# Optimization experiments

Measured on AMD Instinct MI355X. Metric: run time of the kernel, lower is better.

## Reference

```python
import jax, jax.numpy as jnp
import numpy as np

B, N, D = 2, 4096, 512
H, DH = 8, 64  # heads, dim_head; inner_dim = H*DH = 512
SCALE = DH ** -0.5


def setup_inputs() -> dict:
    key = jax.random.key(0)
    ks = jax.random.split(key, 5)
    s = 0.02
    return {
        "x": jax.random.normal(ks[0], (B, N, D), dtype=jnp.float32),
        "Wq": jax.random.normal(ks[1], (D, H * DH), dtype=jnp.float32) * s,
        "Wk": jax.random.normal(ks[2], (D, H * DH), dtype=jnp.float32) * s,
        "Wv": jax.random.normal(ks[3], (D, H * DH), dtype=jnp.float32) * s,
        "Wo": jax.random.normal(ks[4], (H * DH, D), dtype=jnp.float32) * s,
        "bo": jnp.zeros((D,), dtype=jnp.float32),
    }


def reference(x, Wq, Wk, Wv, Wo, bo):
    b, n, _ = x.shape
    # projections (bias-free), then split heads: b n (h d) -> b h n d
    q = (x @ Wq).reshape(b, n, H, DH).transpose(0, 2, 1, 3)
    k = (x @ Wk).reshape(b, n, H, DH).transpose(0, 2, 1, 3)
    v = (x @ Wv).reshape(b, n, H, DH).transpose(0, 2, 1, 3)
    # fp32 QK^T (module upcasts under ATTN_PRECISION='fp32')
    sim = jnp.einsum("bhid,bhjd->bhij", q.astype(jnp.float32), k.astype(jnp.float32)) * SCALE
    attn = jax.nn.softmax(sim, axis=-1)
    out = jnp.einsum("bhij,bhjd->bhid", attn, v)
    # merge heads: b h n d -> b n (h d)
    out = out.transpose(0, 2, 1, 3).reshape(b, n, H * DH)
    return out @ Wo + bo  # dropout p=0 -> identity
```

## Files before the change

### kernel.cpp

```cpp
#include <hip/hip_runtime.h>


typedef __bf16 bf16;
typedef __bf16 bf16x2 __attribute__((ext_vector_type(2)));
typedef __bf16 bf16x4 __attribute__((ext_vector_type(4)));
typedef __bf16 bf16x8 __attribute__((ext_vector_type(8)));
typedef float  f32x2  __attribute__((ext_vector_type(2)));
typedef float  f32x4  __attribute__((ext_vector_type(4)));
typedef float  f32x16 __attribute__((ext_vector_type(16)));

#define MFMA16 __builtin_amdgcn_mfma_f32_16x16x32_bf16
#define MFMA32 __builtin_amdgcn_mfma_f32_32x32x16_bf16

__device__ __forceinline__ int swz(int b) { return b ^ ((b >> 3) & 0x70); }

__device__ __forceinline__ void gload16(const void* g, void* l) {
  __builtin_amdgcn_global_load_lds(
      (const __attribute__((address_space(1))) unsigned int*)g,
      (__attribute__((address_space(3))) unsigned int*)l, 16, 0, 0);
}

__device__ __forceinline__ unsigned pk2(float a, float b) {
  union { bf16x2 h; unsigned u; } x;
  x.h[0] = (bf16)a; x.h[1] = (bf16)b;
  return x.u;
}

__global__ __launch_bounds__(256) void k_cvt(const float* __restrict__ x,
                                             const float* __restrict__ Wq,
                                             const float* __restrict__ Wk,
                                             const float* __restrict__ Wv,
                                             const float* __restrict__ Wo,
                                             bf16* __restrict__ xb,
                                             bf16* __restrict__ Wts) {
  int bid = blockIdx.x;
  if (bid < 4096) {
    int i = (bid * 256 + threadIdx.x) * 4;
    f32x4 v = *(const f32x4*)(x + i);
    bf16x4 o;
    o[0] = (bf16)v[0]; o[1] = (bf16)v[1]; o[2] = (bf16)v[2]; o[3] = (bf16)v[3];
    *(bf16x4*)(xb + i) = o;
  } else {
    int t = (bid - 4096) * 256 + threadIdx.x;
    int w = t >> 18, idx = t & 262143;
    int k = idx >> 9, n = idx & 511;
    const float* W = (w == 0) ? Wq : (w == 1) ? Wk : (w == 2) ? Wv : Wo;
    Wts[(size_t)w * 262144 + n * 512 + k] = (bf16)W[k * 512 + n];
  }
}

__device__ __forceinline__ void gemm_mainloop(const char* Ag, const char* Bg,
                                              char* sA, char* sB, f32x4 acc[4][4]) {
  const int tid = threadIdx.x;
  const int g = (tid >> 4) & 3, lr = tid & 15;
  const int wr = ((tid >> 7) & 1) * 64, wc = ((tid >> 6) & 1) * 64;
  f32x4 zero = {0.f, 0.f, 0.f, 0.f};
#pragma unroll
  for (int mt = 0; mt < 4; mt++)
#pragma unroll
    for (int nt = 0; nt < 4; nt++) acc[mt][nt] = zero;

  for (int k0 = 0; k0 < 512; k0 += 64) {
#pragma unroll
    for (int i = 0; i < 4; i++) {
      int c = i * 256 + tid;
      int row = c >> 3, cl = (c & 7) ^ (row & 7);
      gload16(Ag + row * 1024 + k0 * 2 + cl * 16, sA + (c & ~63) * 16);
    }
#pragma unroll
    for (int i = 0; i < 4; i++) {
      int c = i * 256 + tid;
      int row = c >> 3, cl = (c & 7) ^ (row & 7);
      gload16(Bg + row * 1024 + k0 * 2 + cl * 16, sB + (c & ~63) * 16);
    }
    __syncthreads();
#pragma unroll
    for (int kk = 0; kk < 2; kk++) {
      bf16x8 af[4], bfr[4];
#pragma unroll
      for (int mt = 0; mt < 4; mt++)
        af[mt] = *(const bf16x8*)(sA + swz((wr + mt * 16 + lr) * 128 + kk * 64 + g * 16));
#pragma unroll
      for (int nt = 0; nt < 4; nt++)
        bfr[nt] = *(const bf16x8*)(sB + swz((wc + nt * 16 + lr) * 128 + kk * 64 + g * 16));
#pragma unroll
      for (int mt = 0; mt < 4; mt++)
#pragma unroll
        for (int nt = 0; nt < 4; nt++)
          acc[mt][nt] = MFMA16(af[mt], bfr[nt], acc[mt][nt], 0, 0, 0);
    }
    __syncthreads();
  }
}

__global__ __launch_bounds__(256) void k_gemm_qkv(const bf16* __restrict__ Xb,
                                                  const bf16* __restrict__ Wts,
                                                  bf16* __restrict__ Qo,
                                                  bf16* __restrict__ Ko,
                                                  bf16* __restrict__ Vto) {
  __shared__ __align__(16) char smem[32768];
  const int tid = threadIdx.x;
  const int g = (tid >> 4) & 3, lr = tid & 15;
  const int mb = blockIdx.x * 128, nb = blockIdx.y * 128;
  const int mode = blockIdx.z;
  f32x4 acc[4][4];
  gemm_mainloop((const char*)Xb + (size_t)mb * 1024,
                (const char*)(Wts + (size_t)mode * 262144) + (size_t)nb * 1024,
                smem, smem + 16384, acc);
  const int wr = ((tid >> 7) & 1) * 64, wc = ((tid >> 6) & 1) * 64;
  const float qs = 0.18033688011112042f;
#pragma unroll
  for (int mt = 0; mt < 4; mt++)
#pragma unroll
    for (int nt = 0; nt < 4; nt++)
#pragma unroll
      for (int r = 0; r < 4; r++) {
        int m = mb + wr + mt * 16 + g * 4 + r;
        int cc = nb + wc + nt * 16 + lr;
        float v = acc[mt][nt][r];
        int b = m >> 12, ns = m & 4095, h = cc >> 6, d = cc & 63;
        if (mode == 0)
          Qo[((size_t)(b * 8 + h) * 4096 + ns) * 64 + d] = (bf16)(v * qs);
        else if (mode == 1)
          Ko[((size_t)(b * 8 + h) * 4096 + ns) * 64 + d] = (bf16)v;
        else
          Vto[((size_t)(b * 8 + h) * 64 + d) * 4096 + ns] = (bf16)v;
      }
}

__global__ __launch_bounds__(256) void k_gemm_out(const bf16* __restrict__ Ob,
                                                  const bf16* __restrict__ WtO,
                                                  const float* __restrict__ bo,
                                                  float* __restrict__ out) {
  __shared__ __align__(16) char smem[32768];
  const int tid = threadIdx.x;
  const int g = (tid >> 4) & 3, lr = tid & 15;
  const int mb = blockIdx.x * 128, nb = blockIdx.y * 128;
  f32x4 acc[4][4];
  gemm_mainloop((const char*)Ob + (size_t)mb * 1024,
                (const char*)WtO + (size_t)nb * 1024, smem, smem + 16384, acc);
  const int wr = ((tid >> 7) & 1) * 64, wc = ((tid >> 6) & 1) * 64;
#pragma unroll
  for (int mt = 0; mt < 4; mt++)
#pragma unroll
    for (int nt = 0; nt < 4; nt++)
#pragma unroll
      for (int r = 0; r < 4; r++) {
        int m = mb + wr + mt * 16 + g * 4 + r;
        int cc = nb + wc + nt * 16 + lr;
        out[(size_t)m * 512 + cc] = acc[mt][nt][r] + bo[cc];
      }
}

__global__ __launch_bounds__(512, 4) void k_attn(const bf16* __restrict__ Q,
                                                 const bf16* __restrict__ K,
                                                 const bf16* __restrict__ Vt,
                                                 bf16* __restrict__ O) {
  __shared__ __align__(16) char smem[65536];
  const int tid = threadIdx.x;
  const int l = tid & 63, w = tid >> 6, lo = l & 31, hi = l >> 5;
  const int strip = w & 3, half = w >> 2;
  const int tid2 = tid & 255;
  const int bh = blockIdx.y;
  const int q0 = blockIdx.x * 128 + strip * 32;
  const char* Qp = (const char*)Q + ((size_t)bh * 4096 + q0 + lo) * 128;
  bf16x8 qf[4];
#pragma unroll
  for (int ks = 0; ks < 4; ks++) qf[ks] = *(const bf16x8*)(Qp + ks * 32 + hi * 16);

  const int srow = tid2 >> 3, scl = (tid2 & 7) ^ (srow & 7);
  const char* pK0 = (const char*)K + (size_t)bh * 4096 * 128 +
                    (size_t)half * 2048 * 128 + srow * 128 + scl * 16;
  const char* pV0 = (const char*)Vt + (size_t)bh * 64 * 8192 +
                    (size_t)half * 4096 + (size_t)srow * 8192 + scl * 16;
  char* lbase = smem + half * 32768;
  const int sdst = (tid2 & ~63) * 16;

  const int offR = swz(lo * 128 + hi * 16);

  f32x16 acc0 = {0.f}, acc1 = {0.f};
  float mrun = -3.0e38f, lsum = 0.f;

  {
    char* d = lbase + sdst;
    gload16(pK0, d);
    gload16(pK0 + 4096, d + 4096);
    gload16(pV0, d + 8192);
    gload16(pV0 + 262144, d + 12288);
  }
  pK0 += 8192; pV0 += 128;
  __syncthreads();

  for (int t = 0; t < 32; t++) {
    if (t < 31) {
      char* d = lbase + ((t + 1) & 1) * 16384 + sdst;
      gload16(pK0, d);
      gload16(pK0 + 4096, d + 4096);
      gload16(pV0, d + 8192);
      gload16(pV0 + 262144, d + 12288);
      pK0 += 8192; pV0 += 128;
    }
    const char* b0 = lbase + (t & 1) * 16384;
    const char* pk_[4] = {b0 + offR, b0 + (offR ^ 32), b0 + (offR ^ 64),
                          b0 + (offR ^ 96)};
    f32x16 s0v = {0.f}, s1v = {0.f};
    __builtin_amdgcn_s_setprio(1);
#pragma unroll
    for (int ks = 0; ks < 4; ks++) {
      bf16x8 kf0 = *(const bf16x8*)(pk_[ks]);
      bf16x8 kf1 = *(const bf16x8*)(pk_[ks] + 4096);
      s0v = MFMA32(kf0, qf[ks], s0v, 0, 0, 0);
      s1v = MFMA32(kf1, qf[ks], s1v, 0, 0, 0);
    }
    __builtin_amdgcn_s_setprio(0);
    union C16 { f32x16 v; f32x2 d[8]; float f[16]; };
    C16 S0, S1; S0.v = s0v; S1.v = s1v;
    f32x2 t8[8];
#pragma unroll
    for (int r = 0; r < 8; r++) t8[r] = __builtin_elementwise_max(S0.d[r], S1.d[r]);
#pragma unroll
    for (int r = 0; r < 4; r++) t8[r] = __builtin_elementwise_max(t8[r], t8[r + 4]);
    t8[0] = __builtin_elementwise_max(t8[0], t8[2]);
    t8[1] = __builtin_elementwise_max(t8[1], t8[3]);
    t8[0] = __builtin_elementwise_max(t8[0], t8[1]);
    float pmax = fmaxf(t8[0][0], t8[0][1]);
    pmax = fmaxf(pmax, __shfl_xor(pmax, 32, 64));
    if (t == 0) {
      mrun = pmax;
    } else if (!__all(pmax - mrun <= 8.0f)) {
      float mnew = fmaxf(mrun, pmax);
      float alpha = __builtin_amdgcn_exp2f(mrun - mnew);
      lsum *= alpha;
#pragma unroll
      for (int r = 0; r < 16; r++) {
        float af = __shfl(alpha, (r & 3) + 8 * (r >> 2) + 4 * hi, 64);
        acc0[r] *= af; acc1[r] *= af;
      }
      mrun = mnew;
    }
    const f32x2 mb2 = {mrun, mrun};
#pragma unroll
    for (int r = 0; r < 8; r++) { S0.d[r] -= mb2; S1.d[r] -= mb2; }
#pragma unroll
    for (int r = 0; r < 16; r++) {
      S0.f[r] = __builtin_amdgcn_exp2f(S0.f[r]);
      S1.f[r] = __builtin_amdgcn_exp2f(S1.f[r]);
    }
    f32x2 sa[8];
#pragma unroll
    for (int r = 0; r < 8; r++) sa[r] = S0.d[r] + S1.d[r];
#pragma unroll
    for (int r = 0; r < 4; r++) sa[r] += sa[r + 4];
    sa[0] += sa[2]; sa[1] += sa[3]; sa[0] += sa[1];
    float rs = sa[0][0] + sa[0][1];
    rs += __shfl_xor(rs, 32, 64);
    lsum += rs;
    union U8 { unsigned u[4]; bf16x8 v; };
    bf16x8 pa[4];
#pragma unroll
    for (int j = 0; j < 4; j++) {
      const float* sp = (j < 2) ? S0.f : S1.f;
      int base = (j & 1) * 8;
      unsigned A0 = pk2(sp[base + 0], sp[base + 1]), A1 = pk2(sp[base + 2], sp[base + 3]);
      unsigned B0 = pk2(sp[base + 4], sp[base + 5]), B1 = pk2(sp[base + 6], sp[base + 7]);
      asm("v_permlane32_swap_b32 %0, %1" : "+v"(A0), "+v"(B0));
      asm("v_permlane32_swap_b32 %0, %1" : "+v"(A1), "+v"(B1));
      U8 pu;
      pu.u[0] = A0; pu.u[1] = A1; pu.u[2] = B0; pu.u[3] = B1;
      pa[j] = pu.v;
    }
    __builtin_amdgcn_s_setprio(1);
#pragma unroll
    for (int ks = 0; ks < 4; ks++) {
      bf16x8 vf0 = *(const bf16x8*)(pk_[ks] + 8192);
      bf16x8 vf1 = *(const bf16x8*)(pk_[ks] + 12288);
      acc0 = MFMA32(pa[ks], vf0, acc0, 0, 0, 0);
      acc1 = MFMA32(pa[ks], vf1, acc1, 0, 0, 0);
    }
    __builtin_amdgcn_s_setprio(0);
    __syncthreads();
  }
  float* accStash = (float*)smem;
  float* mArr = (float*)(smem + 32768);
  float* lArr = (float*)(smem + 36864);
  float* cArr = (float*)(smem + 40960);
  if (l < 32) { mArr[w * 32 + lo] = mrun; lArr[w * 32 + lo] = lsum; }
  __syncthreads();
  if (l < 32) {
    float mP = mArr[(w ^ 4) * 32 + lo];
    float lP = lArr[(w ^ 4) * 32 + lo];
    float mn = fmaxf(mrun, mP);
    float wS = __builtin_amdgcn_exp2f(mrun - mn);
    float wP = __builtin_amdgcn_exp2f(mP - mn);
    cArr[w * 32 + lo] = wS / (lsum * wS + lP * wP);
  }
  __syncthreads();
  if (half == 1) {
#pragma unroll
    for (int r = 0; r < 16; r++) {
      int qrow = (r & 3) + 8 * (r >> 2) + 4 * hi;
      float cf = cArr[w * 32 + qrow];
      accStash[(strip * 32 + qrow) * 64 + lo] = acc0[r] * cf;
      accStash[(strip * 32 + qrow) * 64 + lo + 32] = acc1[r] * cf;
    }
  }
  __syncthreads();
  if (half == 0) {
    const int b = bh >> 3, h = bh & 7;
#pragma unroll
    for (int r = 0; r < 16; r++) {
      int qrow = (r & 3) + 8 * (r >> 2) + 4 * hi;
      float cf = cArr[w * 32 + qrow];
      float o0 = acc0[r] * cf + accStash[(strip * 32 + qrow) * 64 + lo];
      float o1 = acc1[r] * cf + accStash[(strip * 32 + qrow) * 64 + lo + 32];
      size_t base = ((size_t)b * 4096 + q0 + qrow) * 512 + h * 64 + lo;
      O[base] = (bf16)o0;
      O[base + 32] = (bf16)o1;
    }
  }
}

extern "C" void kernel_launch(void* const* d_in, const int* in_sizes, int n_in,
                              void* d_out, int out_size, void* d_ws, size_t ws_size,
                              hipStream_t stream) {
  (void)in_sizes; (void)n_in; (void)out_size; (void)ws_size;
  const float* x  = (const float*)d_in[0];
  const float* Wq = (const float*)d_in[1];
  const float* Wk = (const float*)d_in[2];
  const float* Wv = (const float*)d_in[3];
  const float* Wo = (const float*)d_in[4];
  const float* bo = (const float*)d_in[5];
  float* out = (float*)d_out;
  char* ws = (char*)d_ws;
  bf16* Xb  = (bf16*)(ws);
  bf16* Wts = (bf16*)(ws + 8388608);
  bf16* Qb  = (bf16*)(ws + 10485760);
  bf16* Kb  = (bf16*)(ws + 18874368);
  bf16* Vtb = (bf16*)(ws + 27262976);
  bf16* Ob  = (bf16*)(ws + 35651584);

  hipLaunchKernelGGL(k_cvt, dim3(8192), dim3(256), 0, stream,
                     x, Wq, Wk, Wv, Wo, Xb, Wts);
  hipLaunchKernelGGL(k_gemm_qkv, dim3(64, 4, 3), dim3(256), 0, stream,
                     Xb, Wts, Qb, Kb, Vtb);
  hipLaunchKernelGGL(k_attn, dim3(32, 16), dim3(512), 0, stream, Qb, Kb, Vtb, Ob);
  hipLaunchKernelGGL(k_gemm_out, dim3(64, 4), dim3(256), 0, stream,
                     Ob, Wts + 3 * 262144, bo, out);
}
```

Baseline: 149.9 us.

## Software-pipeline attention loop so QK^T of next tile overlaps softmax of current

```diff
diff --git a/kernel.cpp b/kernel.cpp
--- a/kernel.cpp
+++ b/kernel.cpp
@@ -152,7 +152,7 @@
       }
 }
 
-__global__ __launch_bounds__(512, 4) void k_attn(const bf16* __restrict__ Q,
+__global__ __launch_bounds__(512, 3) void k_attn(const bf16* __restrict__ Q,
                                                  const bf16* __restrict__ K,
                                                  const bf16* __restrict__ Vt,
                                                  bf16* __restrict__ O) {
@@ -169,52 +169,42 @@
   for (int ks = 0; ks < 4; ks++) qf[ks] = *(const bf16x8*)(Qp + ks * 32 + hi * 16);
 
   const int srow = tid2 >> 3, scl = (tid2 & 7) ^ (srow & 7);
-  const char* pK0 = (const char*)K + (size_t)bh * 4096 * 128 +
-                    (size_t)half * 2048 * 128 + srow * 128 + scl * 16;
-  const char* pV0 = (const char*)Vt + (size_t)bh * 64 * 8192 +
-                    (size_t)half * 4096 + (size_t)srow * 8192 + scl * 16;
-  char* lbase = smem + half * 32768;
+  const char* pK = (const char*)K + (size_t)bh * 4096 * 128 +
+                   (size_t)half * 2048 * 128 + srow * 128 + scl * 16;
+  const char* pV = (const char*)Vt + (size_t)bh * 64 * 8192 +
+                   (size_t)half * 4096 + (size_t)srow * 8192 + scl * 16;
+  char* hb = smem + half * 32768;
   const int sdst = (tid2 & ~63) * 16;
+  char* dK0 = hb + sdst;
+  char* dK1 = hb + 8192 + sdst;
+  char* dV0 = hb + 16384 + sdst;
+  char* dV1 = hb + 24576 + sdst;
+  const char* rK0 = hb;
+  const char* rK1 = hb + 8192;
+  const char* rV0 = hb + 16384;
+  const char* rV1 = hb + 24576;
 
   const int offR = swz(lo * 128 + hi * 16);
 
-  f32x16 acc0 = {0.f}, acc1 = {0.f};
-  float mrun = -3.0e38f, lsum = 0.f;
-
-  {
-    char* d = lbase + sdst;
-    gload16(pK0, d);
-    gload16(pK0 + 4096, d + 4096);
-    gload16(pV0, d + 8192);
-    gload16(pV0 + 262144, d + 12288);
-  }
-  pK0 += 8192; pV0 += 128;
-  __syncthreads();
-
-  for (int t = 0; t < 32; t++) {
-    if (t < 31) {
-      char* d = lbase + ((t + 1) & 1) * 16384 + sdst;
-      gload16(pK0, d);
-      gload16(pK0 + 4096, d + 4096);
-      gload16(pV0, d + 8192);
-      gload16(pV0 + 262144, d + 12288);
-      pK0 += 8192; pV0 += 128;
-    }
-    const char* b0 = lbase + (t & 1) * 16384;
-    const char* pk_[4] = {b0 + offR, b0 + (offR ^ 32), b0 + (offR ^ 64),
-                          b0 + (offR ^ 96)};
-    f32x16 s0v = {0.f}, s1v = {0.f};
+  f32x16 acc0 = {}, acc1 = {};
+  float mrun = -1.0e30f, lsum = 0.f;
+
+  auto QKI = [&](const char* kb, f32x16& s0v, f32x16& s1v) {
     __builtin_amdgcn_s_setprio(1);
+    s0v = f32x16{}; s1v = f32x16{};
 #pragma unroll
     for (int ks = 0; ks < 4; ks++) {
-      bf16x8 kf0 = *(const bf16x8*)(pk_[ks]);
-      bf16x8 kf1 = *(const bf16x8*)(pk_[ks] + 4096);
+      bf16x8 kf0 = *(const bf16x8*)(kb + (offR ^ (ks * 32)));
+      bf16x8 kf1 = *(const bf16x8*)(kb + 4096 + (offR ^ (ks * 32)));
       s0v = MFMA32(kf0, qf[ks], s0v, 0, 0, 0);
       s1v = MFMA32(kf1, qf[ks], s1v, 0, 0, 0);
     }
     __builtin_amdgcn_s_setprio(0);
+  };
+
+  auto SM = [&](f32x16& s0r, f32x16& s1r, bf16x8* pa) {
     union C16 { f32x16 v; f32x2 d[8]; float f[16]; };
-    C16 S0, S1; S0.v = s0v; S1.v = s1v;
+    C16 S0, S1; S0.v = s0r; S1.v = s1r;
     f32x2 t8[8];
 #pragma unroll
     for (int r = 0; r < 8; r++) t8[r] = __builtin_elementwise_max(S0.d[r], S1.d[r]);
@@ -225,9 +215,7 @@
     t8[0] = __builtin_elementwise_max(t8[0], t8[1]);
     float pmax = fmaxf(t8[0][0], t8[0][1]);
     pmax = fmaxf(pmax, __shfl_xor(pmax, 32, 64));
-    if (t == 0) {
-      mrun = pmax;
-    } else if (!__all(pmax - mrun <= 8.0f)) {
+    if (!__all(pmax - mrun <= 8.0f)) {
       float mnew = fmaxf(mrun, pmax);
       float alpha = __builtin_amdgcn_exp2f(mrun - mnew);
       lsum *= alpha;
@@ -256,7 +244,6 @@
     rs += __shfl_xor(rs, 32, 64);
     lsum += rs;
     union U8 { unsigned u[4]; bf16x8 v; };
-    bf16x8 pa[4];
 #pragma unroll
     for (int j = 0; j < 4; j++) {
       const float* sp = (j < 2) ? S0.f : S1.f;
@@ -269,17 +256,55 @@
       pu.u[0] = A0; pu.u[1] = A1; pu.u[2] = B0; pu.u[3] = B1;
       pa[j] = pu.v;
     }
+  };
+
+  auto PVS = [&](const bf16x8* pa, const char* vb) {
     __builtin_amdgcn_s_setprio(1);
 #pragma unroll
     for (int ks = 0; ks < 4; ks++) {
-      bf16x8 vf0 = *(const bf16x8*)(pk_[ks] + 8192);
-      bf16x8 vf1 = *(const bf16x8*)(pk_[ks] + 12288);
+      bf16x8 vf0 = *(const bf16x8*)(vb + (offR ^ (ks * 32)));
+      bf16x8 vf1 = *(const bf16x8*)(vb + 4096 + (offR ^ (ks * 32)));
       acc0 = MFMA32(pa[ks], vf0, acc0, 0, 0, 0);
       acc1 = MFMA32(pa[ks], vf1, acc1, 0, 0, 0);
     }
     __builtin_amdgcn_s_setprio(0);
+  };
+
+  gload16(pK, dK0); gload16(pK + 4096, dK0 + 4096); pK += 8192;
+  gload16(pK, dK1); gload16(pK + 4096, dK1 + 4096); pK += 8192;
+  gload16(pV, dV0); gload16(pV + 262144, dV0 + 4096); pV += 128;
+  __syncthreads();
+
+  f32x16 SA0, SA1, SB0, SB1;
+  QKI(rK0, SA0, SA1);
+
+  for (int t = 0; t < 32; t += 2) {
+    QKI(rK1, SB0, SB1);
+    if (t + 2 < 32) {
+      gload16(pK, dK0); gload16(pK + 4096, dK0 + 4096); pK += 8192;
+    }
+    gload16(pV, dV1); gload16(pV + 262144, dV1 + 4096); pV += 128;
+    {
+      bf16x8 pa[4];
+      SM(SA0, SA1, pa);
+      PVS(pa, rV0);
+    }
     __syncthreads();
-  }
+    if (t + 2 < 32) QKI(rK0, SA0, SA1);
+    if (t + 3 < 32) {
+      gload16(pK, dK1); gload16(pK + 4096, dK1 + 4096); pK += 8192;
+    }
+    if (t + 2 < 32) {
+      gload16(pV, dV0); gload16(pV + 262144, dV0 + 4096); pV += 128;
+    }
+    {
+      bf16x8 pa[4];
+      SM(SB0, SB1, pa);
+      PVS(pa, rV1);
+    }
+    __syncthreads();
+  }
+
   float* accStash = (float*)smem;
   float* mArr = (float*)(smem + 32768);
   float* lArr = (float*)(smem + 36864);
```

After: 180.5 us. 1.2x slower.
